# Kernel tuning notes

Hardware: AMD Instinct MI355X
Metric: run time of the kernel (lower is better)

The kernel has to match this reference:

```python
import jax, jax.numpy as jnp
import numpy as np

N = 50000
D_IN = 128
D_OUT = 128
EPS = 1e-5


def setup_inputs() -> dict:
    key = jax.random.key(0)
    ks = jax.random.split(key, 10)
    x = jax.random.normal(ks[0], (N, D_IN), dtype=jnp.float32)
    edge_index = jax.random.randint(ks[1], (2, 800000), 0, N, dtype=jnp.int64)
    s_in = 1.0 / np.sqrt(D_IN)
    s_out = 1.0 / np.sqrt(D_OUT)
    return {
        "x": x,
        "edge_index": edge_index,
        # SAGEConv 1: lin_l (on aggregated neighbors, with bias), lin_r (root, no bias)
        "w1_l": jax.random.uniform(ks[2], (D_OUT, D_IN), jnp.float32, -s_in, s_in),
        "b1_l": jnp.zeros((D_OUT,), jnp.float32),
        "w1_r": jax.random.uniform(ks[3], (D_OUT, D_IN), jnp.float32, -s_in, s_in),
        # SAGEConv 2
        "w2_l": jax.random.uniform(ks[4], (D_OUT, D_OUT), jnp.float32, -s_out, s_out),
        "b2_l": jnp.zeros((D_OUT,), jnp.float32),
        "w2_r": jax.random.uniform(ks[5], (D_OUT, D_OUT), jnp.float32, -s_out, s_out),
        # BatchNorm affine params
        "bn_gamma": jnp.ones((D_OUT,), jnp.float32),
        "bn_beta": jnp.zeros((D_OUT,), jnp.float32),
    }


def _sage_conv(x, src, dst, w_l, b_l, w_r):
    # mean aggregation of source-node features into target nodes
    msg = x[src]                                              # [E, D]
    agg = jax.ops.segment_sum(msg, dst, num_segments=N)       # [N, D]
    cnt = jax.ops.segment_sum(jnp.ones((src.shape[0],), x.dtype), dst, num_segments=N)
    mean = agg / jnp.maximum(cnt, 1.0)[:, None]
    return mean @ w_l.T + b_l + x @ w_r.T


def _batch_norm(x, gamma, beta):
    mu = jnp.mean(x, axis=0)
    var = jnp.mean(jnp.square(x - mu), axis=0)  # biased, as in torch BN training
    return (x - mu) * jax.lax.rsqrt(var + EPS) * gamma + beta


def reference(x, edge_index, w1_l, b1_l, w1_r, w2_l, b2_l, w2_r, bn_gamma, bn_beta):
    src, dst = edge_index[0], edge_index[1]
    h = _sage_conv(x, src, dst, w1_l, b1_l, w1_r)
    h = _batch_norm(h, bn_gamma, bn_beta)
    h = jax.nn.relu(h)
    out = _sage_conv(h, src, dst, w2_l, b2_l, w2_r)
    return out
```

## Files before the change

### kernel.cpp

```cpp
#include <hip/hip_runtime.h>

#define D 128
#define EPS 1e-5f
#define FB_EPB 8

typedef unsigned int uint;
typedef __attribute__((ext_vector_type(4))) float f32x4;
typedef __attribute__((ext_vector_type(8))) short s16x8;

__device__ __forceinline__ uint pack_bf16(float a, float b)
{
    uint ua = __float_as_uint(a);
    uint ub = __float_as_uint(b);
    ua += 0x7FFFu + ((ua >> 16) & 1u);
    ub += 0x7FFFu + ((ub >> 16) & 1u);
    return (ua >> 16) | (ub & 0xFFFF0000u);
}
__device__ __forceinline__ float bf_lo(uint v) { return __uint_as_float(v << 16); }
__device__ __forceinline__ float bf_hi(uint v) { return __uint_as_float(v & 0xFFFF0000u); }

__global__ void prep_kernel(const float* __restrict__ x, uint* __restrict__ xb, int ncvt,
                            const float* __restrict__ w1l, const float* __restrict__ w1r,
                            const float* __restrict__ w2l, const float* __restrict__ w2r,
                            uint* __restrict__ wb1, uint* __restrict__ wb2)
{
    int idx = blockIdx.x * 256 + threadIdx.x;
    if (idx < ncvt) {
        float4 v = ((const float4*)x)[idx];
        uint2 o;
        o.x = pack_bf16(v.x, v.y);
        o.y = pack_bf16(v.z, v.w);
        ((uint2*)xb)[idx] = o;
    } else if (idx < ncvt + 8192) {
        int r = idx - ncvt;
        int layer = r >> 12;
        int rem = r & 4095;
        int lane = rem & 63;
        int knt = rem >> 6;
        int kstep = knt >> 3, nt = knt & 7;
        int nn = nt * 16 + (lane & 15);
        int kbase = kstep * 32 + (lane >> 4) * 8;
        const float* wl = layer ? w2l : w1l;
        const float* wr = layer ? w2r : w1r;
        uint* wb = layer ? wb2 : wb1;
        float v[8];
#pragma unroll
        for (int j = 0; j < 8; j++) {
            int k = kbase + j;
            v[j] = (k < D) ? wl[nn * D + k] : wr[nn * D + (k - D)];
        }
        uint4 o;
        o.x = pack_bf16(v[0], v[1]);
        o.y = pack_bf16(v[2], v[3]);
        o.z = pack_bf16(v[4], v[5]);
        o.w = pack_bf16(v[6], v[7]);
        ((uint4*)wb)[(kstep * 8 + nt) * 64 + lane] = o;
    } else if (idx < ncvt + 8192 + 32) {
        ((uint2*)xb)[ncvt + (idx - ncvt - 8192)] = make_uint2(0, 0);
    }
}

__global__ __launch_bounds__(512) void bcount_kernel(const int* __restrict__ dst,
                                                     int* __restrict__ bcnt,
                                                     int E, int nblk, int nbuck)
{
    __shared__ int cnt[128];
    int t = threadIdx.x;
    if (t < 128) cnt[t] = 0;
    __syncthreads();
    int e0 = blockIdx.x * (512 * FB_EPB);
#pragma unroll
    for (int k = 0; k < FB_EPB; k++) {
        int e = e0 + k * 512 + t;
        if (e < E) atomicAdd(&cnt[dst[e] >> 9], 1);
    }
    __syncthreads();
    if (t < nbuck) bcnt[t * nblk + blockIdx.x] = cnt[t];
}

__global__ __launch_bounds__(1024) void bscan_kernel(int* __restrict__ bcnt, int M)
{
    __shared__ int sums[1024];
    int t = threadIdx.x;
    int chunk = (M + 1023) / 1024;
    int b0 = t * chunk;
    int b1 = min(b0 + chunk, M);
    int s = 0;
    for (int i = b0; i < b1; i++) s += bcnt[i];
    sums[t] = s;
    __syncthreads();
    for (int off = 1; off < 1024; off <<= 1) {
        int u = (t >= off) ? sums[t - off] : 0;
        __syncthreads();
        sums[t] += u;
        __syncthreads();
    }
    int run = sums[t] - s;
    for (int i = b0; i < b1; i++) { int v = bcnt[i]; bcnt[i] = run; run += v; }
    if (t == 1023) bcnt[M] = sums[1023];
}

__global__ __launch_bounds__(512) void bscatter_kernel(const int* __restrict__ src,
                                                       const int* __restrict__ dst,
                                                       const int* __restrict__ bcnt,
                                                       uint2* __restrict__ ebuf,
                                                       int E, int nblk, int nbuck)
{
    __shared__ int cnt[128], base[128];
    int t = threadIdx.x;
    if (t < 128) cnt[t] = 0;
    __syncthreads();
    int e0 = blockIdx.x * (512 * FB_EPB);
    int s[FB_EPB], d[FB_EPB], loc[FB_EPB];
#pragma unroll
    for (int k = 0; k < FB_EPB; k++) {
        int e = e0 + k * 512 + t;
        if (e < E) {
            s[k] = src[e];
            d[k] = dst[e];
            loc[k] = atomicAdd(&cnt[d[k] >> 9], 1);
        }
    }
    __syncthreads();
    if (t < nbuck) base[t] = bcnt[t * nblk + blockIdx.x];
    __syncthreads();
#pragma unroll
    for (int k = 0; k < FB_EPB; k++) {
        int e = e0 + k * 512 + t;
        if (e < E) {
            int b = d[k] >> 9;
            ebuf[base[b] + loc[k]] = make_uint2((uint)s[k], (uint)d[k]);
        }
    }
}

__global__ __launch_bounds__(512) void pbuild_kernel(const int* __restrict__ bcnt,
                                                     const uint2* __restrict__ ebuf,
                                                     int* __restrict__ rowptr,
                                                     int* __restrict__ col,
                                                     int n, int nblk, int nbuck, int M, int E)
{
    __shared__ int lcnt[512], lscan[512];
    int t = threadIdx.x;
    int b = blockIdx.x;
    int nb = b << 9;
    int e0 = bcnt[b * nblk];
    int e1 = (b + 1 < nbuck) ? bcnt[(b + 1) * nblk] : bcnt[M];
    lcnt[t] = 0;
    __syncthreads();
    for (int i = e0 + t; i < e1; i += 512)
        atomicAdd(&lcnt[(int)ebuf[i].y - nb], 1);
    __syncthreads();
    int s = lcnt[t];
    lscan[t] = s;
    __syncthreads();
    for (int off = 1; off < 512; off <<= 1) {
        int u = (t >= off) ? lscan[t - off] : 0;
        __syncthreads();
        lscan[t] += u;
        __syncthreads();
    }
    int start = e0 + lscan[t] - s;
    int ncnt = min(512, n - nb);
    if (t < ncnt) rowptr[nb + t] = start;
    if (b == nbuck - 1 && t == 0) rowptr[n] = E;
    lscan[t] = start;
    __syncthreads();
    for (int i = e0 + t; i < e1; i += 512) {
        uint2 ed = ebuf[i];
        int p = atomicAdd(&lscan[(int)ed.y - nb], 1);
        col[p] = (int)ed.x;
    }
}

__global__ __launch_bounds__(256) void agg_kernel(const int* __restrict__ rowptr,
                                                  const int* __restrict__ col,
                                                  const uint* __restrict__ featb,
                                                  uint* __restrict__ aggb, int n)
{
    int node = blockIdx.x * 4 + (threadIdx.x >> 6);
    if (node >= n) return;
    int lane = threadIdx.x & 63;
    int sub = lane >> 4, l16 = lane & 15;
    int r0 = rowptr[node], r1 = rowptr[node + 1];
    uint4* out4 = (uint4*)aggb;
    if (r0 == r1) {
        if (lane < 16) out4[(size_t)node * 16 + l16] = make_uint4(0, 0, 0, 0);
        return;
    }
    float acc[8] = {0.f, 0.f, 0.f, 0.f, 0.f, 0.f, 0.f, 0.f};
    const uint4* fb = (const uint4*)featb;
    int last = r1 - 1;

    for (int i = r0; i < r1; i += 32) {
        uint4 v[8];
#pragma unroll
        for (int r = 0; r < 8; r++) {
            int idx = i + r * 4 + sub;
            int cl = col[min(idx, last)];
            int c = (idx < r1) ? cl : n;
            v[r] = fb[(size_t)c * 16 + l16];
        }
#pragma unroll
        for (int r = 0; r < 8; r++) {
            uint4 u = v[r];
            acc[0] += bf_lo(u.x); acc[1] += bf_hi(u.x);
            acc[2] += bf_lo(u.y); acc[3] += bf_hi(u.y);
            acc[4] += bf_lo(u.z); acc[5] += bf_hi(u.z);
            acc[6] += bf_lo(u.w); acc[7] += bf_hi(u.w);
        }
    }
#pragma unroll
    for (int j = 0; j < 8; j++) {
        acc[j] += __shfl_down(acc[j], 32);
        acc[j] += __shfl_down(acc[j], 16);
    }
    if (lane < 16) {
        float inv = 1.0f / (float)(r1 - r0);
        uint4 o;
        o.x = pack_bf16(acc[0] * inv, acc[1] * inv);
        o.y = pack_bf16(acc[2] * inv, acc[3] * inv);
        o.z = pack_bf16(acc[4] * inv, acc[5] * inv);
        o.w = pack_bf16(acc[6] * inv, acc[7] * inv);
        out4[(size_t)node * 16 + l16] = o;
    }
}

#define TSTRIDE 132
template<bool FUSE1>
__global__ __launch_bounds__(256) void conv_kernel(
    const uint* __restrict__ p1b, const uint* __restrict__ p2b,
    const uint* __restrict__ wb, const float* __restrict__ bias,
    float* __restrict__ outf, uint* __restrict__ outb,
    float* __restrict__ pstats, int n)
{
    extern __shared__ float smem[];
    float* tile = smem;
    int w = threadIdx.x >> 6, lane = threadIdx.x & 63;
    int quad = lane >> 4, l15 = lane & 15;
    int nb = blockIdx.x * 64;

    const uint4* p1 = (const uint4*)p1b;
    const uint4* p2 = (const uint4*)p2b;
    const uint4* wv = (const uint4*)wb;

    uint4 B[8][2];
    int nt0 = w * 2;
#pragma unroll
    for (int ks = 0; ks < 8; ks++) {
#pragma unroll
        for (int t = 0; t < 2; t++)
            B[ks][t] = wv[(ks * 8 + nt0 + t) * 64 + lane];
    }

    float bv0 = bias[nt0 * 16 + l15];
    float bv1 = bias[nt0 * 16 + 16 + l15];

    for (int rt = 0; rt < 4; rt++) {
        int node = nb + rt * 16 + l15;
        int nc = min(node, n - 1);
        uint4 A[8];
#pragma unroll
        for (int ks = 0; ks < 4; ks++) A[ks] = p1[(size_t)nc * 16 + ks * 4 + quad];
#pragma unroll
        for (int ks = 0; ks < 4; ks++) A[ks + 4] = p2[(size_t)nc * 16 + ks * 4 + quad];

        f32x4 acc0 = {bv0, bv0, bv0, bv0};
        f32x4 acc1 = {bv1, bv1, bv1, bv1};
#pragma unroll
        for (int ks = 0; ks < 8; ks++) {
            s16x8 a = *(s16x8*)&A[ks];
            acc0 = __builtin_amdgcn_mfma_f32_16x16x32_bf16(a, *(s16x8*)&B[ks][0], acc0, 0, 0, 0);
            acc1 = __builtin_amdgcn_mfma_f32_16x16x32_bf16(a, *(s16x8*)&B[ks][1], acc1, 0, 0, 0);
        }
        int row0 = nb + rt * 16 + quad * 4;
        int colbase = nt0 * 16 + l15;
        if (FUSE1) {
            int rloc0 = rt * 16 + quad * 4;
#pragma unroll
            for (int reg = 0; reg < 4; reg++) {
                bool ok = (row0 + reg) < n;
                tile[(rloc0 + reg) * TSTRIDE + colbase]      = ok ? acc0[reg] : 0.f;
                tile[(rloc0 + reg) * TSTRIDE + colbase + 16] = ok ? acc1[reg] : 0.f;
            }
        } else {
#pragma unroll
            for (int reg = 0; reg < 4; reg++) {
                int row = row0 + reg;
                if (row < n) {
                    outf[(size_t)row * D + colbase] = acc0[reg];
                    outf[(size_t)row * D + colbase + 16] = acc1[reg];
                }
            }
        }
    }

    if (FUSE1) {
        __syncthreads();
        int colj = threadIdx.x & 127, half = threadIdx.x >> 7;
        float s = 0.f, ss = 0.f;
        for (int r = half * 32; r < half * 32 + 32; r++) {
            float v = tile[r * TSTRIDE + colj];
            s += v;
            ss += v * v;
        }
        float* pb = pstats + (size_t)blockIdx.x * 512 + half * 256;
        pb[colj] = s;
        pb[128 + colj] = ss;
        uint4* ob4 = (uint4*)outb;
#pragma unroll
        for (int q4 = 0; q4 < 4; q4++) {
            int idx = q4 * 256 + threadIdx.x;
            int r = idx >> 4, q = idx & 15;
            int row = nb + r;
            if (row < n) {
                float* tr = &tile[r * TSTRIDE + q * 8];
                uint4 o;
                o.x = pack_bf16(tr[0], tr[1]);
                o.y = pack_bf16(tr[2], tr[3]);
                o.z = pack_bf16(tr[4], tr[5]);
                o.w = pack_bf16(tr[6], tr[7]);
                ob4[(size_t)row * 16 + q] = o;
            }
        }
    }
}

__global__ __launch_bounds__(256) void reduce_kernel(const float* __restrict__ pstats,
                                                     float* __restrict__ stats,
                                                     int* __restrict__ ctr,
                                                     const float* __restrict__ gamma,
                                                     const float* __restrict__ beta,
                                                     float* __restrict__ scsh,
                                                     int nparts, float n_inv)
{
    __shared__ int lastf;
    int j = threadIdx.x;
    int chunk = (nparts + gridDim.x - 1) / gridDim.x;
    int p0 = blockIdx.x * chunk;
    int p1 = min(p0 + chunk, nparts);
    float s = 0.f;
    for (int p = p0; p < p1; p++) s += pstats[(size_t)p * 256 + j];
    unsafeAtomicAdd(&stats[j], s);
    __threadfence();
    __syncthreads();
    if (threadIdx.x == 0) {
        int old = atomicAdd(ctr, 1);
        lastf = (old == (int)gridDim.x - 1) ? 1 : 0;
    }
    __syncthreads();
    if (lastf && j < 128) {
        float sm = atomicAdd(&stats[j], 0.0f);
        float sq = atomicAdd(&stats[128 + j], 0.0f);
        float mean = sm * n_inv;
        float var = fmaxf(sq * n_inv - mean * mean, 0.f);
        float sc = gamma[j] * rsqrtf(var + EPS);
        scsh[j] = sc;
        scsh[128 + j] = beta[j] - mean * sc;
    }
}

__global__ __launch_bounds__(256) void bnapply_kernel(const uint* __restrict__ hb,
                                                      const float* __restrict__ scsh,
                                                      uint* __restrict__ hbn, int total2)
{
    __shared__ float scs[256];
    scs[threadIdx.x] = scsh[threadIdx.x];
    __syncthreads();
    int idx = blockIdx.x * 256 + threadIdx.x;
    if (blockIdx.x == 0 && threadIdx.x < 32)
        ((uint2*)hbn)[total2 + threadIdx.x] = make_uint2(0, 0);
    if (idx >= total2) return;
    int j4 = (idx & 31) * 4;
    uint2 u = ((const uint2*)hb)[idx];
    float e0 = fmaxf(bf_lo(u.x) * scs[j4 + 0] + scs[128 + j4 + 0], 0.f);
    float e1 = fmaxf(bf_hi(u.x) * scs[j4 + 1] + scs[128 + j4 + 1], 0.f);
    float e2 = fmaxf(bf_lo(u.y) * scs[j4 + 2] + scs[128 + j4 + 2], 0.f);
    float e3 = fmaxf(bf_hi(u.y) * scs[j4 + 3] + scs[128 + j4 + 3], 0.f);
    uint2 o;
    o.x = pack_bf16(e0, e1);
    o.y = pack_bf16(e2, e3);
    ((uint2*)hbn)[idx] = o;
}

extern "C" void kernel_launch(void* const* d_in, const int* in_sizes, int n_in,
                              void* d_out, int out_size, void* d_ws, size_t ws_size,
                              hipStream_t stream)
{
    const float* x     = (const float*)d_in[0];
    const int*   ei    = (const int*)d_in[1];
    const float* w1_l  = (const float*)d_in[2];
    const float* b1_l  = (const float*)d_in[3];
    const float* w1_r  = (const float*)d_in[4];
    const float* w2_l  = (const float*)d_in[5];
    const float* b2_l  = (const float*)d_in[6];
    const float* w2_r  = (const float*)d_in[7];
    const float* gamma = (const float*)d_in[8];
    const float* beta  = (const float*)d_in[9];

    int N = in_sizes[0] / D;
    int E = in_sizes[1] / 2;
    const int* src = ei;
    const int* dst = ei + E;

    int cblocks = (N + 63) / 64;
    int nbuck   = (N + 511) >> 9;
    int nblk    = (E + 4095) / 4096;
    int M       = nbuck * nblk;

    uint*  aggb   = (uint*)d_ws;
    uint*  xb     = aggb + (size_t)N * 64;
    uint*  hb     = xb + (size_t)(N + 1) * 64;
    uint*  hbn    = hb + (size_t)N * 64;
    uint*  wb1    = hbn + (size_t)(N + 1) * 64;
    uint*  wb2    = wb1 + 16384;
    uint2* ebuf   = (uint2*)(wb2 + 16384);
    float* stats  = (float*)(ebuf + E);
    int*   ctr    = (int*)(stats + 256);
    float* scsh   = stats + 260;
    float* pstats = scsh + 256;
    int*   rowptr = (int*)(pstats + (size_t)cblocks * 512);
    int*   col    = rowptr + N + 1;
    int*   bcnt   = col + E;

    hipMemsetAsync(stats, 0, 257 * sizeof(float), stream);

    int ncvt = N * 32;
    int pblocks = (ncvt + 8192 + 32 + 255) / 256;
    prep_kernel<<<pblocks, 256, 0, stream>>>(x, xb, ncvt, w1_l, w1_r, w2_l, w2_r, wb1, wb2);

    int ablocks = (N + 3) / 4;

    bcount_kernel<<<nblk, 512, 0, stream>>>(dst, bcnt, E, nblk, nbuck);
    bscan_kernel<<<1, 1024, 0, stream>>>(bcnt, M);
    bscatter_kernel<<<nblk, 512, 0, stream>>>(src, dst, bcnt, ebuf, E, nblk, nbuck);
    pbuild_kernel<<<nbuck, 512, 0, stream>>>(bcnt, ebuf, rowptr, col, N, nblk, nbuck, M, E);

    agg_kernel<<<ablocks, 256, 0, stream>>>(rowptr, col, xb, aggb, N);
    conv_kernel<true><<<cblocks, 256, 64 * TSTRIDE * 4, stream>>>(
        aggb, xb, wb1, b1_l, nullptr, hb, pstats, N);

    reduce_kernel<<<32, 256, 0, stream>>>(pstats, stats, ctr, gamma, beta, scsh,
                                          cblocks * 2, 1.0f / (float)N);
    bnapply_kernel<<<(N * 32 + 255) / 256, 256, 0, stream>>>(hb, scsh, hbn, N * 32);

    agg_kernel<<<ablocks, 256, 0, stream>>>(rowptr, col, hbn, aggb, N);
    conv_kernel<false><<<cblocks, 256, 1024, stream>>>(
        aggb, hbn, wb2, b2_l, (float*)d_out, nullptr, nullptr, N);
}
```

Before: 266.3 us.

## Fuse prep with bucket count and scan, fold BN-apply into second aggregation

Merges the conversion/prep kernel, the bucket-count kernel and the single-block scan into one launch. The last finishing count block performs the scan, with completion tracked by an atomic counter. Removes the separate BN-apply pass by having the second aggregation apply scale, shift and ReLU on the fly to gathered neighbour rows and also write the normalized root rows. The aggregation unroll depth drops from 8 to 4 loads per iteration. This saves launches and one full pass over h, at the cost of recomputing BN for every gathered edge and fewer loads in flight per wave.

```diff
diff --git a/kernel.cpp b/kernel.cpp
--- a/kernel.cpp
+++ b/kernel.cpp
@@ -19,85 +19,100 @@
 __device__ __forceinline__ float bf_lo(uint v) { return __uint_as_float(v << 16); }
 __device__ __forceinline__ float bf_hi(uint v) { return __uint_as_float(v & 0xFFFF0000u); }
 
-__global__ void prep_kernel(const float* __restrict__ x, uint* __restrict__ xb, int ncvt,
-                            const float* __restrict__ w1l, const float* __restrict__ w1r,
-                            const float* __restrict__ w2l, const float* __restrict__ w2r,
-                            uint* __restrict__ wb1, uint* __restrict__ wb2)
-{
-    int idx = blockIdx.x * 256 + threadIdx.x;
-    if (idx < ncvt) {
-        float4 v = ((const float4*)x)[idx];
-        uint2 o;
-        o.x = pack_bf16(v.x, v.y);
-        o.y = pack_bf16(v.z, v.w);
-        ((uint2*)xb)[idx] = o;
-    } else if (idx < ncvt + 8192) {
-        int r = idx - ncvt;
-        int layer = r >> 12;
-        int rem = r & 4095;
-        int lane = rem & 63;
-        int knt = rem >> 6;
-        int kstep = knt >> 3, nt = knt & 7;
-        int nn = nt * 16 + (lane & 15);
-        int kbase = kstep * 32 + (lane >> 4) * 8;
-        const float* wl = layer ? w2l : w1l;
-        const float* wr = layer ? w2r : w1r;
-        uint* wb = layer ? wb2 : wb1;
-        float v[8];
-#pragma unroll
-        for (int j = 0; j < 8; j++) {
-            int k = kbase + j;
-            v[j] = (k < D) ? wl[nn * D + k] : wr[nn * D + (k - D)];
-        }
-        uint4 o;
-        o.x = pack_bf16(v[0], v[1]);
-        o.y = pack_bf16(v[2], v[3]);
-        o.z = pack_bf16(v[4], v[5]);
-        o.w = pack_bf16(v[6], v[7]);
-        ((uint4*)wb)[(kstep * 8 + nt) * 64 + lane] = o;
-    } else if (idx < ncvt + 8192 + 32) {
-        ((uint2*)xb)[ncvt + (idx - ncvt - 8192)] = make_uint2(0, 0);
-    }
-}
-
-__global__ __launch_bounds__(512) void bcount_kernel(const int* __restrict__ dst,
-                                                     int* __restrict__ bcnt,
-                                                     int E, int nblk, int nbuck)
+__global__ __launch_bounds__(512) void prep_count_kernel(
+    const float* __restrict__ x, uint* __restrict__ xb, int ncvt,
+    const float* __restrict__ w1l, const float* __restrict__ w1r,
+    const float* __restrict__ w2l, const float* __restrict__ w2r,
+    uint* __restrict__ wb1, uint* __restrict__ wb2,
+    const int* __restrict__ dst, int* __restrict__ bcnt,
+    int E, int nblk, int nbuck, int M, int* __restrict__ scanctr)
 {
     __shared__ int cnt[128];
+    __shared__ int sums[512];
+    __shared__ int lastf;
     int t = threadIdx.x;
-    if (t < 128) cnt[t] = 0;
-    __syncthreads();
-    int e0 = blockIdx.x * (512 * FB_EPB);
-#pragma unroll
-    for (int k = 0; k < FB_EPB; k++) {
-        int e = e0 + k * 512 + t;
-        if (e < E) atomicAdd(&cnt[dst[e] >> 9], 1);
-    }
-    __syncthreads();
-    if (t < nbuck) bcnt[t * nblk + blockIdx.x] = cnt[t];
-}
-
-__global__ __launch_bounds__(1024) void bscan_kernel(int* __restrict__ bcnt, int M)
-{
-    __shared__ int sums[1024];
-    int t = threadIdx.x;
-    int chunk = (M + 1023) / 1024;
-    int b0 = t * chunk;
-    int b1 = min(b0 + chunk, M);
-    int s = 0;
-    for (int i = b0; i < b1; i++) s += bcnt[i];
-    sums[t] = s;
-    __syncthreads();
-    for (int off = 1; off < 1024; off <<= 1) {
-        int u = (t >= off) ? sums[t - off] : 0;
-        __syncthreads();
-        sums[t] += u;
-        __syncthreads();
-    }
-    int run = sums[t] - s;
-    for (int i = b0; i < b1; i++) { int v = bcnt[i]; bcnt[i] = run; run += v; }
-    if (t == 1023) bcnt[M] = sums[1023];
+
+    if (blockIdx.x < nblk) {
+        if (t < 128) cnt[t] = 0;
+        __syncthreads();
+        int e0 = blockIdx.x * (512 * FB_EPB);
+#pragma unroll
+        for (int k = 0; k < FB_EPB; k++) {
+            int e = e0 + k * 512 + t;
+            if (e < E) atomicAdd(&cnt[dst[e] >> 9], 1);
+        }
+        __syncthreads();
+        if (t < nbuck) bcnt[t * nblk + blockIdx.x] = cnt[t];
+
+        __syncthreads();
+        if (t == 0) {
+            __threadfence();
+            int old = atomicAdd(scanctr, 1);
+            lastf = (old == nblk - 1) ? 1 : 0;
+            if (lastf) __threadfence();
+        }
+        __syncthreads();
+        if (lastf) {
+            int chunk = (M + 511) / 512;
+            int b0 = t * chunk;
+            int b1 = min(b0 + chunk, M);
+            int s = 0;
+            for (int i = b0; i < b1; i++)
+                s += __hip_atomic_load(&bcnt[i], __ATOMIC_RELAXED,
+                                       __HIP_MEMORY_SCOPE_AGENT);
+            sums[t] = s;
+            __syncthreads();
+            for (int off = 1; off < 512; off <<= 1) {
+                int u = (t >= off) ? sums[t - off] : 0;
+                __syncthreads();
+                sums[t] += u;
+                __syncthreads();
+            }
+            int run = sums[t] - s;
+            for (int i = b0; i < b1; i++) {
+                int v = __hip_atomic_load(&bcnt[i], __ATOMIC_RELAXED,
+                                          __HIP_MEMORY_SCOPE_AGENT);
+                bcnt[i] = run;
+                run += v;
+            }
+            if (t == 511) bcnt[M] = sums[511];
+        }
+    } else {
+        int idx = (blockIdx.x - nblk) * 512 + t;
+        if (idx < ncvt) {
+            float4 v = ((const float4*)x)[idx];
+            uint2 o;
+            o.x = pack_bf16(v.x, v.y);
+            o.y = pack_bf16(v.z, v.w);
+            ((uint2*)xb)[idx] = o;
+        } else if (idx < ncvt + 8192) {
+            int r = idx - ncvt;
+            int layer = r >> 12;
+            int rem = r & 4095;
+            int lane = rem & 63;
+            int knt = rem >> 6;
+            int kstep = knt >> 3, nt = knt & 7;
+            int nn = nt * 16 + (lane & 15);
+            int kbase = kstep * 32 + (lane >> 4) * 8;
+            const float* wl = layer ? w2l : w1l;
+            const float* wr = layer ? w2r : w1r;
+            uint* wb = layer ? wb2 : wb1;
+            float v[8];
+#pragma unroll
+            for (int j = 0; j < 8; j++) {
+                int k = kbase + j;
+                v[j] = (k < D) ? wl[nn * D + k] : wr[nn * D + (k - D)];
+            }
+            uint4 o;
+            o.x = pack_bf16(v[0], v[1]);
+            o.y = pack_bf16(v[2], v[3]);
+            o.z = pack_bf16(v[4], v[5]);
+            o.w = pack_bf16(v[6], v[7]);
+            ((uint4*)wb)[(kstep * 8 + nt) * 64 + lane] = o;
+        } else if (idx < ncvt + 8192 + 32) {
+            ((uint2*)xb)[ncvt + (idx - ncvt - 8192)] = make_uint2(0, 0);
+        }
+    }
 }
 
 __global__ __launch_bounds__(512) void bscatter_kernel(const int* __restrict__ src,
@@ -192,22 +207,110 @@
     const uint4* fb = (const uint4*)featb;
     int last = r1 - 1;
 
-    for (int i = r0; i < r1; i += 32) {
-        uint4 v[8];
-#pragma unroll
-        for (int r = 0; r < 8; r++) {
+    for (int i = r0; i < r1; i += 16) {
+        uint4 v[4];
+#pragma unroll
+        for (int r = 0; r < 4; r++) {
             int idx = i + r * 4 + sub;
             int cl = col[min(idx, last)];
             int c = (idx < r1) ? cl : n;
             v[r] = fb[(size_t)c * 16 + l16];
         }
 #pragma unroll
-        for (int r = 0; r < 8; r++) {
+        for (int r = 0; r < 4; r++) {
             uint4 u = v[r];
             acc[0] += bf_lo(u.x); acc[1] += bf_hi(u.x);
             acc[2] += bf_lo(u.y); acc[3] += bf_hi(u.y);
             acc[4] += bf_lo(u.z); acc[5] += bf_hi(u.z);
             acc[6] += bf_lo(u.w); acc[7] += bf_hi(u.w);
+        }
+    }
+#pragma unroll
+    for (int j = 0; j < 8; j++) {
+        acc[j] += __shfl_down(acc[j], 32);
+        acc[j] += __shfl_down(acc[j], 16);
+    }
+    if (lane < 16) {
+        float inv = 1.0f / (float)(r1 - r0);
+        uint4 o;
+        o.x = pack_bf16(acc[0] * inv, acc[1] * inv);
+        o.y = pack_bf16(acc[2] * inv, acc[3] * inv);
+        o.z = pack_bf16(acc[4] * inv, acc[5] * inv);
+        o.w = pack_bf16(acc[6] * inv, acc[7] * inv);
+        out4[(size_t)node * 16 + l16] = o;
+    }
+}
+
+__global__ __launch_bounds__(256) void aggbn_kernel(const int* __restrict__ rowptr,
+                                                    const int* __restrict__ col,
+                                                    const uint* __restrict__ hb,
+                                                    uint* __restrict__ aggb,
+                                                    uint* __restrict__ hbn,
+                                                    const float* __restrict__ scsh, int n)
+{
+    int node = blockIdx.x * 4 + (threadIdx.x >> 6);
+    if (node >= n) return;
+    int lane = threadIdx.x & 63;
+    int sub = lane >> 4, l16 = lane & 15;
+    const uint4* fb = (const uint4*)hb;
+    uint4* out4 = (uint4*)aggb;
+    uint4* hbn4 = (uint4*)hbn;
+
+    float4 sca = *(const float4*)&scsh[l16 * 8];
+    float4 scb = *(const float4*)&scsh[l16 * 8 + 4];
+    float4 sha = *(const float4*)&scsh[128 + l16 * 8];
+    float4 shb = *(const float4*)&scsh[128 + l16 * 8 + 4];
+    float sc[8] = {sca.x, sca.y, sca.z, sca.w, scb.x, scb.y, scb.z, scb.w};
+    float sh[8] = {sha.x, sha.y, sha.z, sha.w, shb.x, shb.y, shb.z, shb.w};
+
+    if (lane < 16) {
+        uint4 u = fb[(size_t)node * 16 + l16];
+        float e0 = fmaxf(fmaf(bf_lo(u.x), sc[0], sh[0]), 0.f);
+        float e1 = fmaxf(fmaf(bf_hi(u.x), sc[1], sh[1]), 0.f);
+        float e2 = fmaxf(fmaf(bf_lo(u.y), sc[2], sh[2]), 0.f);
+        float e3 = fmaxf(fmaf(bf_hi(u.y), sc[3], sh[3]), 0.f);
+        float e4 = fmaxf(fmaf(bf_lo(u.z), sc[4], sh[4]), 0.f);
+        float e5 = fmaxf(fmaf(bf_hi(u.z), sc[5], sh[5]), 0.f);
+        float e6 = fmaxf(fmaf(bf_lo(u.w), sc[6], sh[6]), 0.f);
+        float e7 = fmaxf(fmaf(bf_hi(u.w), sc[7], sh[7]), 0.f);
+        uint4 o;
+        o.x = pack_bf16(e0, e1);
+        o.y = pack_bf16(e2, e3);
+        o.z = pack_bf16(e4, e5);
+        o.w = pack_bf16(e6, e7);
+        hbn4[(size_t)node * 16 + l16] = o;
+    }
+
+    int r0 = rowptr[node], r1 = rowptr[node + 1];
+    if (r0 == r1) {
+        if (lane < 16) out4[(size_t)node * 16 + l16] = make_uint4(0, 0, 0, 0);
+        return;
+    }
+    float acc[8] = {0.f, 0.f, 0.f, 0.f, 0.f, 0.f, 0.f, 0.f};
+    int last = r1 - 1;
+
+    for (int i = r0; i < r1; i += 16) {
+        uint4 v[4];
+        float m[4];
+#pragma unroll
+        for (int r = 0; r < 4; r++) {
+            int idx = i + r * 4 + sub;
+            int cl = col[min(idx, last)];
+            m[r] = (idx < r1) ? 1.f : 0.f;
+            v[r] = fb[(size_t)cl * 16 + l16];
+        }
+#pragma unroll
+        for (int r = 0; r < 4; r++) {
+            uint4 u = v[r];
+            float mr = m[r];
+            acc[0] = fmaf(mr, fmaxf(fmaf(bf_lo(u.x), sc[0], sh[0]), 0.f), acc[0]);
+            acc[1] = fmaf(mr, fmaxf(fmaf(bf_hi(u.x), sc[1], sh[1]), 0.f), acc[1]);
+            acc[2] = fmaf(mr, fmaxf(fmaf(bf_lo(u.y), sc[2], sh[2]), 0.f), acc[2]);
+            acc[3] = fmaf(mr, fmaxf(fmaf(bf_hi(u.y), sc[3], sh[3]), 0.f), acc[3]);
+            acc[4] = fmaf(mr, fmaxf(fmaf(bf_lo(u.z), sc[4], sh[4]), 0.f), acc[4]);
+            acc[5] = fmaf(mr, fmaxf(fmaf(bf_hi(u.z), sc[5], sh[5]), 0.f), acc[5]);
+            acc[6] = fmaf(mr, fmaxf(fmaf(bf_lo(u.w), sc[6], sh[6]), 0.f), acc[6]);
+            acc[7] = fmaf(mr, fmaxf(fmaf(bf_hi(u.w), sc[7], sh[7]), 0.f), acc[7]);
         }
     }
 #pragma unroll
@@ -360,29 +463,6 @@
     }
 }
 
-__global__ __launch_bounds__(256) void bnapply_kernel(const uint* __restrict__ hb,
-                                                      const float* __restrict__ scsh,
-                                                      uint* __restrict__ hbn, int total2)
-{
-    __shared__ float scs[256];
-    scs[threadIdx.x] = scsh[threadIdx.x];
-    __syncthreads();
-    int idx = blockIdx.x * 256 + threadIdx.x;
-    if (blockIdx.x == 0 && threadIdx.x < 32)
-        ((uint2*)hbn)[total2 + threadIdx.x] = make_uint2(0, 0);
-    if (idx >= total2) return;
-    int j4 = (idx & 31) * 4;
-    uint2 u = ((const uint2*)hb)[idx];
-    float e0 = fmaxf(bf_lo(u.x) * scs[j4 + 0] + scs[128 + j4 + 0], 0.f);
-    float e1 = fmaxf(bf_hi(u.x) * scs[j4 + 1] + scs[128 + j4 + 1], 0.f);
-    float e2 = fmaxf(bf_lo(u.y) * scs[j4 + 2] + scs[128 + j4 + 2], 0.f);
-    float e3 = fmaxf(bf_hi(u.y) * scs[j4 + 3] + scs[128 + j4 + 3], 0.f);
-    uint2 o;
-    o.x = pack_bf16(e0, e1);
-    o.y = pack_bf16(e2, e3);
-    ((uint2*)hbn)[idx] = o;
-}
-
 extern "C" void kernel_launch(void* const* d_in, const int* in_sizes, int n_in,
                               void* d_out, int out_size, void* d_ws, size_t ws_size,
                               hipStream_t stream)
@@ -412,39 +492,41 @@
     uint*  xb     = aggb + (size_t)N * 64;
     uint*  hb     = xb + (size_t)(N + 1) * 64;
     uint*  hbn    = hb + (size_t)N * 64;
-    uint*  wb1    = hbn + (size_t)(N + 1) * 64;
+    uint*  wb1    = hbn + (size_t)N * 64;
     uint*  wb2    = wb1 + 16384;
     uint2* ebuf   = (uint2*)(wb2 + 16384);
     float* stats  = (float*)(ebuf + E);
-    int*   ctr    = (int*)(stats + 256);
-    float* scsh   = stats + 260;
+    int*   scanctr= (int*)(stats + 256);
+    int*   redctr = scanctr + 1;
+    float* scsh   = stats + 258;
     float* pstats = scsh + 256;
     int*   rowptr = (int*)(pstats + (size_t)cblocks * 512);
     int*   col    = rowptr + N + 1;
     int*   bcnt   = col + E;
 
-    hipMemsetAsync(stats, 0, 257 * sizeof(float), stream);
+    hipMemsetAsync(stats, 0, 258 * sizeof(float), stream);
 
     int ncvt = N * 32;
-    int pblocks = (ncvt + 8192 + 32 + 255) / 256;
-    prep_kernel<<<pblocks, 256, 0, stream>>>(x, xb, ncvt, w1_l, w1_r, w2_l, w2_r, wb1, wb2);
-
-    int ablocks = (N + 3) / 4;
-
-    bcount_kernel<<<nblk, 512, 0, stream>>>(dst, bcnt, E, nblk, nbuck);
-    bscan_kernel<<<1, 1024, 0, stream>>>(bcnt, M);
+    int total0 = ncvt + 8192 + 32;
+    int pblocks = (total0 + 511) / 512;
+    prep_count_kernel<<<nblk + pblocks, 512, 0, stream>>>(
+        x, xb, ncvt, w1_l, w1_r, w2_l, w2_r, wb1, wb2,
+        dst, bcnt, E, nblk, nbuck, M, scanctr);
+
     bscatter_kernel<<<nblk, 512, 0, stream>>>(src, dst, bcnt, ebuf, E, nblk, nbuck);
     pbuild_kernel<<<nbuck, 512, 0, stream>>>(bcnt, ebuf, rowptr, col, N, nblk, nbuck, M, E);
+
+    int ablocks = (N + 3) / 4;
 
     agg_kernel<<<ablocks, 256, 0, stream>>>(rowptr, col, xb, aggb, N);
     conv_kernel<true><<<cblocks, 256, 64 * TSTRIDE * 4, stream>>>(
         aggb, xb, wb1, b1_l, nullptr, hb, pstats, N);
 
-    reduce_kernel<<<32, 256, 0, stream>>>(pstats, stats, ctr, gamma, beta, scsh,
+    reduce_kernel<<<32, 256, 0, stream>>>(pstats, stats, redctr, gamma, beta, scsh,
                                           cblocks * 2, 1.0f / (float)N);
-    bnapply_kernel<<<(N * 32 + 255) / 256, 256, 0, stream>>>(hb, scsh, hbn, N * 32);
-
-    agg_kernel<<<ablocks, 256, 0, stream>>>(rowptr, col, hbn, aggb, N);
+
+    aggbn_kernel<<<ablocks, 256, 0, stream>>>(rowptr, col, hb, aggb, hbn, scsh, N);
+
     conv_kernel<false><<<cblocks, 256, 1024, stream>>>(
         aggb, hbn, wb2, b2_l, (float*)d_out, nullptr, nullptr, N);
 }
```

New measurement: 299.4 us. 1.12x slower.
